# Kernel tuning notes

Measured on AMD Instinct MI355X. Metric: run time of the kernel, lower is better.

The kernel has to match this reference:

```python
import jax, jax.numpy as jnp
import numpy as np
import math

NUM_BINS = 10
TAIL_BOUND = 5.0
FILTER_CHANNELS = 192
KERNEL_SIZE = 3
N_LAYERS = 3
HALF = 1
MIN_BIN = 1e-3
MIN_DERIV = 1e-3


def conv1d(x, w, b, dilation=1, groups=1, padding=0):
    # x: [B,C,T], w: [O, C//groups, K]
    y = jax.lax.conv_general_dilated(
        x, w, window_strides=(1,), padding=[(padding, padding)],
        rhs_dilation=(dilation,), dimension_numbers=('NCH', 'OIH', 'NCH'),
        feature_group_count=groups)
    return y + b[None, :, None]


def ln_channels(x, g, b, eps=1e-5):
    # LayerNorm over channel dim (VITS modules.LayerNorm)
    m = jnp.mean(x, axis=1, keepdims=True)
    v = jnp.mean((x - m) ** 2, axis=1, keepdims=True)
    return g[None, :, None] * (x - m) * jax.lax.rsqrt(v + eps) + b[None, :, None]


def rq_spline(x1, uw, uh, ud):
    # piecewise rational-quadratic transform with linear tails (Durkan et al.)
    # x1: [B,1,T]; uw,uh: [B,1,T,K]; ud: [B,1,T,K-1]
    K = NUM_BINS
    tb = TAIL_BOUND
    inside = (x1 >= -tb) & (x1 <= tb)

    const = math.log(math.exp(1.0 - MIN_DERIV) - 1.0)  # softplus^-1(1-min_d)
    ud = jnp.pad(ud, [(0, 0)] * (ud.ndim - 1) + [(1, 1)], constant_values=const)

    widths = jax.nn.softmax(uw, axis=-1)
    widths = MIN_BIN + (1.0 - MIN_BIN * K) * widths
    cumw = jnp.pad(jnp.cumsum(widths, -1), [(0, 0)] * (uw.ndim - 1) + [(1, 0)])
    cumw = 2.0 * tb * cumw - tb
    cumw = cumw.at[..., 0].set(-tb).at[..., -1].set(tb)
    widths = cumw[..., 1:] - cumw[..., :-1]

    heights = jax.nn.softmax(uh, axis=-1)
    heights = MIN_BIN + (1.0 - MIN_BIN * K) * heights
    cumh = jnp.pad(jnp.cumsum(heights, -1), [(0, 0)] * (uh.ndim - 1) + [(1, 0)])
    cumh = 2.0 * tb * cumh - tb
    cumh = cumh.at[..., 0].set(-tb).at[..., -1].set(tb)
    heights = cumh[..., 1:] - cumh[..., :-1]

    derivs = MIN_DERIV + jax.nn.softplus(ud)  # [..., K+1]

    xin = jnp.clip(x1, -tb, tb)  # clamp so out-of-range lanes stay finite
    locs = cumw.at[..., -1].add(1e-6)
    bin_idx = jnp.clip(jnp.sum((xin[..., None] >= locs).astype(jnp.int32), -1) - 1, 0, K - 1)

    def take(a):
        return jnp.take_along_axis(a, bin_idx[..., None], axis=-1)[..., 0]

    icw = take(cumw)
    iw = take(widths)
    ich = take(cumh)
    ih = take(heights)
    d_l = take(derivs[..., :-1])
    d_r = take(derivs[..., 1:])
    delta = ih / iw

    theta = (xin - icw) / iw
    t1m = theta * (1.0 - theta)
    numerator = ih * (delta * theta * theta + d_l * t1m)
    denominator = delta + (d_l + d_r - 2.0 * delta) * t1m
    y = ich + numerator / denominator
    dnum = (delta * delta) * (d_r * theta * theta + 2.0 * delta * t1m + d_l * (1.0 - theta) ** 2)
    lad = jnp.log(dnum) - 2.0 * jnp.log(denominator)

    out = jnp.where(inside, y, x1)       # linear tails: identity outside
    lad = jnp.where(inside, lad, 0.0)
    return out, lad


def reference(x, x_mask, pre_w, pre_b, sep_w, sep_b, pw_w, pw_b,
              ln1_g, ln1_b, ln2_g, ln2_b, proj_w, proj_b):
    x0, x1 = x[:, :HALF], x[:, HALF:]
    h = conv1d(x0, pre_w, pre_b)
    # DDSConv (dilated depth-separable conv stack), p_dropout=0
    for i in range(N_LAYERS):
        d = KERNEL_SIZE ** i
        pad = (KERNEL_SIZE * d - d) // 2
        y = conv1d(h * x_mask, sep_w[i], sep_b[i], dilation=d,
                   groups=FILTER_CHANNELS, padding=pad)
        y = jax.nn.gelu(ln_channels(y, ln1_g[i], ln1_b[i]), approximate=False)
        y = conv1d(y, pw_w[i], pw_b[i])
        y = jax.nn.gelu(ln_channels(y, ln2_g[i], ln2_b[i]), approximate=False)
        h = h + y
    h = h * x_mask
    h = conv1d(h, proj_w, proj_b) * x_mask  # [B, half*(3K-1), T]
    b, c, t = x0.shape
    h = h.reshape(b, c, -1, t).transpose(0, 1, 3, 2)  # [B, half, T, 3K-1]
    scale = math.sqrt(FILTER_CHANNELS)
    uw = h[..., :NUM_BINS] / scale
    uh = h[..., NUM_BINS:2 * NUM_BINS] / scale
    ud = h[..., 2 * NUM_BINS:]
    x1o, lad = rq_spline(x1, uw, uh, ud)
    out = jnp.concatenate([x0, x1o], axis=1) * x_mask
    logdet = jnp.sum(lad * x_mask, axis=(1, 2))
    return out, logdet


def setup_inputs() -> dict:
    key = jax.random.key(0)
    ks = jax.random.split(key, 8)
    B, T, C, L, K = 64, 4096, FILTER_CHANNELS, N_LAYERS, KERNEL_SIZE
    return {
        'x': jax.random.normal(ks[0], (B, 2, T), jnp.float32),
        'x_mask': jnp.ones((B, 1, T), jnp.float32),
        'pre_w': jax.random.normal(ks[1], (C, 1, 1), jnp.float32) * 0.1,
        'pre_b': jnp.zeros((C,), jnp.float32),
        'sep_w': jax.random.normal(ks[2], (L, C, 1, K), jnp.float32) * 0.1,
        'sep_b': jnp.zeros((L, C), jnp.float32),
        'pw_w': jax.random.normal(ks[3], (L, C, C, 1), jnp.float32) * (1.0 / np.sqrt(C).astype(np.float32)),
        'pw_b': jnp.zeros((L, C), jnp.float32),
        'ln1_g': jnp.ones((L, C), jnp.float32),
        'ln1_b': jnp.zeros((L, C), jnp.float32),
        'ln2_g': jnp.ones((L, C), jnp.float32),
        'ln2_b': jnp.zeros((L, C), jnp.float32),
        'proj_w': jax.random.normal(ks[4], (HALF * (3 * NUM_BINS - 1), C, 1), jnp.float32) * 0.01,
        'proj_b': jnp.zeros((HALF * (3 * NUM_BINS - 1),), jnp.float32),
    }
```

## Files before the change

### kernel.cpp

```cpp
#include <hip/hip_runtime.h>
#include <stdint.h>

#define TT_ 4096
#define CC_ 192
#define TILE_ 64
#define HALO_ 13
#define TW_ 90
#define HS_ 100
#define YTS_ 200
#define NT_ 512

typedef float f32x4 __attribute__((ext_vector_type(4)));
typedef short s16x4 __attribute__((ext_vector_type(4)));
typedef short s16x8 __attribute__((ext_vector_type(8)));
typedef uint32_t ui32x2 __attribute__((ext_vector_type(2)));
typedef uint32_t ui32x4 __attribute__((ext_vector_type(4)));

__device__ __forceinline__ float bf2f(short s){
  uint32_t u = ((uint32_t)(uint16_t)s) << 16;
  float f; __builtin_memcpy(&f, &u, 4); return f;
}
__device__ __forceinline__ float bfhalf(uint32_t u, int hi){
  uint32_t v = hi ? (u & 0xFFFF0000u) : (u << 16);
  float f; __builtin_memcpy(&f, &v, 4); return f;
}
__device__ __forceinline__ short f2bf(float f){
  uint32_t u; __builtin_memcpy(&u, &f, 4);
  u += 0x7FFFu + ((u >> 16) & 1u);
  return (short)(u >> 16);
}
__device__ __forceinline__ uint32_t fbits(float f){
  uint32_t u; __builtin_memcpy(&u, &f, 4); return u;
}
__device__ __forceinline__ uint32_t pk_trunc(float lo, float hi){
  return __builtin_amdgcn_perm(fbits(hi), fbits(lo), 0x07060302u);
}
__device__ __forceinline__ uint32_t rne_u(float f){
  uint32_t u = fbits(f);
  return u + 0x7FFFu + ((u >> 16) & 1u);
}
__device__ __forceinline__ uint32_t pk_rne(float lo, float hi){
  return __builtin_amdgcn_perm(rne_u(hi), rne_u(lo), 0x07060302u);
}
__device__ __forceinline__ float gelu_f(float x){
  float t = x*x;
  float p = x*__builtin_fmaf(t, 0.0713548162f, 1.5957691216f);
  float e = __expf(-p);
  return x * __builtin_amdgcn_rcpf(1.0f + e);
}
__device__ __forceinline__ int ytix(int row, int col){
  return row*YTS_ + ((((col >> 3) ^ (row & 3)) << 3) | (col & 7));
}

template<int D>
__device__ __forceinline__ void dw_pass(const short* __restrict__ Hs, short* __restrict__ YTs,
    const float* __restrict__ sw, const float* __restrict__ sb,
    int jlo, int jhi, int tid){
  constexpr int WO = (D==9) ? 16 : 8;
  constexpr int NU = (D==9) ? 20 : 12;
  for (int g = tid; g < 96*12; g += NT_){
    int cg = g % 96, jg = g / 96;
    int j0 = jg*8;
    if (j0 + 8 <= jlo || j0 >= jhi) continue;
    int c0 = cg*2;
    uint32_t wpa[NU], wpb[NU];
    {
      const uint32_t* ra = (const uint32_t*)(Hs + (c0+0)*HS_ + j0 - WO);
      const uint32_t* rb = (const uint32_t*)(Hs + (c0+1)*HS_ + j0 - WO);
      #pragma unroll
      for (int u = 0; u < NU/2; ++u){
        ui32x2 ta = *(const ui32x2*)(ra + u*2);
        ui32x2 tb = *(const ui32x2*)(rb + u*2);
        wpa[u*2] = ta[0]; wpa[u*2+1] = ta[1];
        wpb[u*2] = tb[0]; wpb[u*2+1] = tb[1];
      }
    }
    float w0a = sw[c0*3+0], w1a = sw[c0*3+1], w2a = sw[c0*3+2], bav = sb[c0];
    float w0b = sw[c0*3+3], w1b = sw[c0*3+4], w2b = sw[c0*3+5], bbv = sb[c0+1];
    #pragma unroll
    for (int j = 0; j < 8; ++j){
      int h0 = WO + j - D, h1 = WO + j, h2 = WO + j + D;
      float va = __builtin_fmaf(w0a, bfhalf(wpa[h0>>1], h0&1),
                 __builtin_fmaf(w1a, bfhalf(wpa[h1>>1], h1&1),
                 __builtin_fmaf(w2a, bfhalf(wpa[h2>>1], h2&1), bav)));
      float vb = __builtin_fmaf(w0b, bfhalf(wpb[h0>>1], h0&1),
                 __builtin_fmaf(w1b, bfhalf(wpb[h1>>1], h1&1),
                 __builtin_fmaf(w2b, bfhalf(wpb[h2>>1], h2&1), bbv)));
      *(uint32_t*)(YTs + ytix(j0+j, c0)) = pk_trunc(va, vb);
    }
  }
}

__device__ __forceinline__ void ln_stats(const short* __restrict__ YTs, float* __restrict__ SM,
                                         float* __restrict__ SR, int jlo, int jhi, int tid){
  if (tid < 384){
    int row = tid >> 2, qtr = tid & 3;
    if (row >= jlo && row < jhi){
      float s0 = 0.f, s1 = 0.f, q0 = 0.f, q1 = 0.f;
      #pragma unroll
      for (int u=0;u<6;++u){
        s16x8 v = *(const s16x8*)(YTs + ytix(row, qtr*48 + u*8));
        #pragma unroll
        for (int e=0;e<4;e++){ float f=bf2f(v[e]); s0 += f; q0 = __builtin_fmaf(f,f,q0); }
        #pragma unroll
        for (int e=4;e<8;e++){ float f=bf2f(v[e]); s1 += f; q1 = __builtin_fmaf(f,f,q1); }
      }
      float s = s0+s1, q = q0+q1;
      s += __shfl_xor(s,1); q += __shfl_xor(q,1);
      s += __shfl_xor(s,2); q += __shfl_xor(q,2);
      if (qtr==0){
        float mean = s*(1.f/192.f);
        float var = fmaxf(q*(1.f/192.f) - mean*mean, 0.f);
        SM[row]=mean; SR[row]=rsqrtf(var+1e-5f);
      }
    }
  }
}

__global__ __launch_bounds__(512, 4)
void convflow_main(
    const float* __restrict__ x, const float* __restrict__ xmask,
    const float* __restrict__ pre_w, const float* __restrict__ pre_b,
    const float* __restrict__ sep_w, const float* __restrict__ sep_b,
    const float* __restrict__ pw_b,
    const float* __restrict__ ln1_g, const float* __restrict__ ln1_b,
    const float* __restrict__ ln2_g, const float* __restrict__ ln2_b,
    const float* __restrict__ proj_b,
    const short* __restrict__ Wbf, const short* __restrict__ Pbf,
    float* __restrict__ out, float* __restrict__ part)
{
  __shared__ __align__(16) char smem_raw[78592];
  float* MB = (float*)(smem_raw + 0);
  float* XB = (float*)(smem_raw + 640);
  float* SM = (float*)(smem_raw + 1024);
  float* SR = (float*)(smem_raw + 1408);
  short* H  = (short*)(smem_raw + 1792);
  short* YT = (short*)(smem_raw + 40192);
  float* HP = (float*)(smem_raw + 65792);

  const int tid = threadIdx.x;
  const int b = blockIdx.y, tile = blockIdx.x;
  const int t0 = tile*TILE_ - HALO_;

  for (int idx = tid; idx < 160; idx += NT_){
    int j = idx - 16; int t = t0 + j;
    float m = 0.f;
    if (j >= 0 && j < TW_ && t >= 0 && t < TT_) m = xmask[b*TT_ + t];
    MB[idx] = m;
  }
  if (tid < 96){
    int t = t0 + tid; float v = 0.f;
    if (tid < TW_ && t >= 0 && t < TT_) v = x[(b*2)*TT_ + t];
    XB[tid] = v;
  }
  __syncthreads();

  for (int g = tid; g < CC_*24; g += NT_){
    int jq = g % 24, c = g / 24;
    float w = pre_w[c], bb = pre_b[c];
    int j0 = jq*4;
    float v0 = (w*XB[j0+0] + bb)*MB[16+j0+0];
    float v1 = (w*XB[j0+1] + bb)*MB[16+j0+1];
    float v2 = (w*XB[j0+2] + bb)*MB[16+j0+2];
    float v3 = (w*XB[j0+3] + bb)*MB[16+j0+3];
    ui32x2 o; o[0] = pk_rne(v0, v1); o[1] = pk_rne(v2, v3);
    *(ui32x2*)(H + c*HS_ + j0) = o;
  }
  __syncthreads();

  #pragma unroll 1
  for (int li = 0; li < 3; ++li){
    const int jlo = (li==0) ? 1 : ((li==1) ? 4 : 13);
    const int jhi = (li==0) ? 89 : ((li==1) ? 86 : 77);
    const float* sw = sep_w + li*CC_*3;
    const float* sb = sep_b + li*CC_;

    if (li == 0)      dw_pass<1>(H, YT, sw, sb, jlo, jhi, tid);
    else if (li == 1) dw_pass<3>(H, YT, sw, sb, jlo, jhi, tid);
    else              dw_pass<9>(H, YT, sw, sb, jlo, jhi, tid);
    __syncthreads();

    ln_stats(YT, SM, SR, jlo, jhi, tid); __syncthreads();

    {
      const float* g1 = ln1_g + li*CC_;
      const float* b1 = ln1_b + li*CC_;
      for (int g = tid; g < 96*24; g += NT_){
        int ch = g % 24, row = g / 24;
        short* p = YT + ytix(row, ch*8);
        if (row >= jlo && row < jhi){
          float m = SM[row], r = SR[row];
          s16x8 v = *(s16x8*)p;
          f32x4 ga = *(const f32x4*)&g1[ch*8], gb = *(const f32x4*)&g1[ch*8+4];
          f32x4 ba = *(const f32x4*)&b1[ch*8], bb = *(const f32x4*)&b1[ch*8+4];
          float ov[8];
          #pragma unroll
          for (int e=0;e<4;e++){
            float val = (bf2f(v[e]) - m)*r*ga[e] + ba[e];
            ov[e] = gelu_f(val);
          }
          #pragma unroll
          for (int e=4;e<8;e++){
            float val = (bf2f(v[e]) - m)*r*gb[e-4] + bb[e-4];
            ov[e] = gelu_f(val);
          }
          ui32x4 o;
          #pragma unroll
          for (int e=0;e<4;e++) o[e] = pk_trunc(ov[2*e], ov[2*e+1]);
          *(ui32x4*)p = o;
        } else {
          ui32x4 z = {0u,0u,0u,0u};
          *(ui32x4*)p = z;
        }
      }
    }
    __syncthreads();

    {
      int w = tid >> 6, lane = tid & 63, l16 = lane & 15, q = lane >> 4;
      int Mh = w & 3, Nh = w >> 2;
      f32x4 acc[3][3];
      #pragma unroll
      for (int r=0;r<3;r++)
        #pragma unroll
        for (int s=0;s<3;s++){ f32x4 z = {0.f,0.f,0.f,0.f}; acc[r][s] = z; }
      const short* Wl = Wbf + li*CC_*CC_;
      #pragma unroll
      for (int kk=0;kk<6;++kk){
        s16x8 bv[3], av[3];
        #pragma unroll
        for (int s=0;s<3;++s)
          bv[s] = *(const s16x8*)&YT[ytix((Nh*3+s)*16 + l16, kk*32 + q*8)];
        #pragma unroll
        for (int r=0;r<3;++r)
          av[r] = *(const s16x8*)&Wl[((Mh*3+r)*16 + l16)*CC_ + kk*32 + q*8];
        #pragma unroll
        for (int r=0;r<3;++r)
          #pragma unroll
          for (int s=0;s<3;++s)
            acc[r][s] = __builtin_amdgcn_mfma_f32_16x16x32_bf16(av[r], bv[s], acc[r][s], 0, 0, 0);
      }
      __syncthreads();
      #pragma unroll
      for (int r=0;r<3;++r){
        int m0 = (Mh*3+r)*16 + q*4;
        f32x4 bias = *(const f32x4*)&pw_b[li*CC_ + m0];
        #pragma unroll
        for (int s=0;s<3;++s){
          int n = (Nh*3+s)*16 + l16;
          ui32x2 ov;
          ov[0] = pk_trunc(acc[r][s][0]+bias[0], acc[r][s][1]+bias[1]);
          ov[1] = pk_trunc(acc[r][s][2]+bias[2], acc[r][s][3]+bias[3]);
          *(ui32x2*)(YT + ytix(n, m0)) = ov;
        }
      }
      __syncthreads();
    }

    ln_stats(YT, SM, SR, jlo, jhi, tid); __syncthreads();

    {
      const float* g2 = ln2_g + li*CC_;
      const float* b2 = ln2_b + li*CC_;
      for (int g = tid; g < 24*48; g += NT_){
        int cgp = g % 48, jg = g / 48;
        int j0 = jg*4, c0 = cgp*4;
        if (j0 + 4 <= jlo || j0 >= jhi) continue;
        f32x4 mv = *(f32x4*)&SM[j0], rv = *(f32x4*)&SR[j0];
        f32x4 mk = *(f32x4*)&MB[16 + j0];
        f32x4 gv = *(const f32x4*)&g2[c0], bv = *(const f32x4*)&b2[c0];
        s16x4 yr[4];
        #pragma unroll
        for (int jj=0;jj<4;++jj) yr[jj] = *(s16x4*)(YT + ytix(j0+jj, c0));
        #pragma unroll
        for (int cc=0;cc<4;++cc){
          short* hp_ = H + (c0+cc)*HS_ + j0;
          s16x4 hv = *(s16x4*)hp_;
          float hf[4];
          #pragma unroll
          for (int jj=0;jj<4;++jj){
            int j = j0 + jj;
            float val = (bf2f(yr[jj][cc]) - mv[jj])*rv[jj]*gv[cc] + bv[cc];
            float hn = (bf2f(hv[jj]) + gelu_f(val))*mk[jj];
            bool ok = (j >= jlo) && (j < jhi);
            hf[jj] = ok ? hn : bf2f(hv[jj]);
          }
          ui32x2 o; o[0] = pk_rne(hf[0], hf[1]); o[1] = pk_rne(hf[2], hf[3]);
          *(ui32x2*)hp_ = o;
        }
      }
    }
    __syncthreads();
  }

  {
    int w = tid >> 6;
    if (w < 4){
      int lane = tid & 63, l16 = lane & 15, q = lane >> 4;
      int mt = w >> 1, ntp = w & 1;
      f32x4 pacc[2];
      { f32x4 z = {0.f,0.f,0.f,0.f}; pacc[0] = z; pacc[1] = z; }
      #pragma unroll
      for (int kk=0;kk<6;++kk){
        s16x8 a = *(const s16x8*)&Pbf[(mt*16 + l16)*CC_ + kk*32 + q*8];
        #pragma unroll
        for (int s=0;s<2;++s){
          int n = (ntp*2+s)*16 + l16;
          s16x8 bvv;
          #pragma unroll
          for (int i=0;i<8;++i)
            bvv[i] = H[(kk*32 + q*8 + i)*HS_ + HALO_ + n];
          pacc[s] = __builtin_amdgcn_mfma_f32_16x16x32_bf16(a, bvv, pacc[s], 0, 0, 0);
        }
      }
      #pragma unroll
      for (int s=0;s<2;++s)
        #pragma unroll
        for (int e=0;e<4;e++){
          int m = mt*16 + q*4 + e;
          if (m < 29){
            int n = (ntp*2+s)*16 + l16;
            HP[n*33 + m] = (pacc[s][e] + proj_b[m]) * MB[16 + HALO_ + n];
          }
        }
    }
  }
  __syncthreads();

  if (tid < 64){
    const int n = tid;
    const int tg = tile*TILE_ + n;
    const float msk = MB[16 + HALO_ + n];
    const float* hp = &HP[n*33];
    const float inv_s = 0.07216878364870323f;
    float uw[10], uh[10], ud9[9];
    #pragma unroll
    for (int k=0;k<10;k++){ uw[k] = hp[k]*inv_s; uh[k] = hp[10+k]*inv_s; }
    #pragma unroll
    for (int k=0;k<9;k++) ud9[k] = hp[20+k];

    float cumw[11], cumh[11];
    {
      float mx = uw[0];
      #pragma unroll
      for (int k=1;k<10;k++) mx = fmaxf(mx, uw[k]);
      float ex[10]; float ss = 0.f;
      #pragma unroll
      for (int k=0;k<10;k++){ ex[k] = __expf(uw[k]-mx); ss += ex[k]; }
      float inv = 1.0f/ss;
      cumw[0] = -5.f; float cw = 0.f;
      #pragma unroll
      for (int k=0;k<10;k++){ float wk = 0.001f + 0.99f*(ex[k]*inv); cw += wk; cumw[k+1] = 10.f*cw - 5.f; }
      cumw[10] = 5.f;
    }
    {
      float mx = uh[0];
      #pragma unroll
      for (int k=1;k<10;k++) mx = fmaxf(mx, uh[k]);
      float ex[10]; float ss = 0.f;
      #pragma unroll
      for (int k=0;k<10;k++){ ex[k] = __expf(uh[k]-mx); ss += ex[k]; }
      float inv = 1.0f/ss;
      cumh[0] = -5.f; float ch = 0.f;
      #pragma unroll
      for (int k=0;k<10;k++){ float hk = 0.001f + 0.99f*(ex[k]*inv); ch += hk; cumh[k+1] = 10.f*ch - 5.f; }
      cumh[10] = 5.f;
    }
    float dv[11];
    dv[0] = 1.0f; dv[10] = 1.0f;
    #pragma unroll
    for (int k=0;k<9;k++){
      float u = ud9[k];
      float sp = (u > 15.f) ? u : log1pf(__expf(u));
      dv[k+1] = 0.001f + sp;
    }

    const float x1 = x[(b*2+1)*TT_ + tg];
    const float xin = fminf(fmaxf(x1, -5.f), 5.f);
    int cnt = 0;
    #pragma unroll
    for (int k=0;k<11;k++){
      float lk = cumw[k] + ((k==10) ? 1e-6f : 0.f);
      cnt += (xin >= lk) ? 1 : 0;
    }
    int bin = cnt - 1;
    bin = (bin < 0) ? 0 : ((bin > 9) ? 9 : bin);

    float icw=0.f, iw=1.f, ich=0.f, ih=1.f, dl=1.f, dr=1.f;
    #pragma unroll
    for (int k=0;k<10;k++){
      if (bin == k){
        icw = cumw[k]; iw = cumw[k+1]-cumw[k];
        ich = cumh[k]; ih = cumh[k+1]-cumh[k];
        dl = dv[k]; dr = dv[k+1];
      }
    }
    float delta = ih/iw;
    float th = (xin - icw)/iw;
    float t1m = th*(1.f-th);
    float num = ih*(delta*th*th + dl*t1m);
    float den = delta + (dl + dr - 2.f*delta)*t1m;
    float yv = ich + num/den;
    float omt = 1.f - th;
    float dnum = delta*delta*(dr*th*th + 2.f*delta*t1m + dl*omt*omt);
    float lad = logf(dnum) - 2.f*logf(den);
    bool inside = (x1 >= -5.f) && (x1 <= 5.f);
    float outv = inside ? yv : x1;
    float ladv = inside ? lad : 0.f;

    out[(b*2)*TT_ + tg]   = x[(b*2)*TT_ + tg] * msk;
    out[(b*2+1)*TT_ + tg] = outv * msk;

    float lsum = ladv * msk;
    #pragma unroll
    for (int off = 32; off > 0; off >>= 1) lsum += __shfl_xor(lsum, off);
    if (tid == 0) part[b*64 + tile] = lsum;
  }
}

__global__ void convflow_pre(const float* __restrict__ pw_w, const float* __restrict__ proj_w,
                             short* __restrict__ Wbf, short* __restrict__ Pbf){
  int idx = blockIdx.x*256 + threadIdx.x;
  if (idx < 110592) Wbf[idx] = f2bf(pw_w[idx]);
  if (idx < 32*192){
    int m = idx / 192, k = idx - m*192;
    Pbf[idx] = (m < 29) ? f2bf(proj_w[m*192 + k]) : (short)0;
  }
}

__global__ void convflow_logdet(const float* __restrict__ part, float* __restrict__ out){
  int bb = threadIdx.x;
  if (bb < 64){
    float s = 0.f;
    for (int k=0;k<64;k++) s += part[bb*64 + k];
    out[524288 + bb] = s;
  }
}

extern "C" void kernel_launch(void* const* d_in, const int* in_sizes, int n_in,
                              void* d_out, int out_size, void* d_ws, size_t ws_size,
                              hipStream_t stream) {
  const float* x      = (const float*)d_in[0];
  const float* xmask  = (const float*)d_in[1];
  const float* pre_w  = (const float*)d_in[2];
  const float* pre_b  = (const float*)d_in[3];
  const float* sep_w  = (const float*)d_in[4];
  const float* sep_b  = (const float*)d_in[5];
  const float* pw_w   = (const float*)d_in[6];
  const float* pw_b   = (const float*)d_in[7];
  const float* ln1_g  = (const float*)d_in[8];
  const float* ln1_b  = (const float*)d_in[9];
  const float* ln2_g  = (const float*)d_in[10];
  const float* ln2_b  = (const float*)d_in[11];
  const float* proj_w = (const float*)d_in[12];
  const float* proj_b = (const float*)d_in[13];

  short* Wbf = (short*)d_ws;
  short* Pbf = (short*)((char*)d_ws + 221184);
  float* part = (float*)((char*)d_ws + 233472);
  float* out = (float*)d_out;

  convflow_pre<<<432, 256, 0, stream>>>(pw_w, proj_w, Wbf, Pbf);
  dim3 grid(64, 64);
  convflow_main<<<grid, NT_, 0, stream>>>(x, xmask, pre_w, pre_b, sep_w, sep_b, pw_b,
                                          ln1_g, ln1_b, ln2_g, ln2_b, proj_b,
                                          Wbf, Pbf, out, part);
  convflow_logdet<<<1, 64, 0, stream>>>(part, out);
}
```

Measured before the change: 591.8 us.

## Store residual H tile time-major with swizzled layout for vectorized access

```diff
diff --git a/kernel.cpp b/kernel.cpp
--- a/kernel.cpp
+++ b/kernel.cpp
@@ -6,7 +6,6 @@
 #define TILE_ 64
 #define HALO_ 13
 #define TW_ 90
-#define HS_ 100
 #define YTS_ 200
 #define NT_ 512
 
@@ -20,10 +19,6 @@
   uint32_t u = ((uint32_t)(uint16_t)s) << 16;
   float f; __builtin_memcpy(&f, &u, 4); return f;
 }
-__device__ __forceinline__ float bfhalf(uint32_t u, int hi){
-  uint32_t v = hi ? (u & 0xFFFF0000u) : (u << 16);
-  float f; __builtin_memcpy(&f, &v, 4); return f;
-}
 __device__ __forceinline__ short f2bf(float f){
   uint32_t u; __builtin_memcpy(&u, &f, 4);
   u += 0x7FFFu + ((u >> 16) & 1u);
@@ -56,38 +51,29 @@
 __device__ __forceinline__ void dw_pass(const short* __restrict__ Hs, short* __restrict__ YTs,
     const float* __restrict__ sw, const float* __restrict__ sb,
     int jlo, int jhi, int tid){
-  constexpr int WO = (D==9) ? 16 : 8;
-  constexpr int NU = (D==9) ? 20 : 12;
-  for (int g = tid; g < 96*12; g += NT_){
-    int cg = g % 96, jg = g / 96;
-    int j0 = jg*8;
-    if (j0 + 8 <= jlo || j0 >= jhi) continue;
-    int c0 = cg*2;
-    uint32_t wpa[NU], wpb[NU];
-    {
-      const uint32_t* ra = (const uint32_t*)(Hs + (c0+0)*HS_ + j0 - WO);
-      const uint32_t* rb = (const uint32_t*)(Hs + (c0+1)*HS_ + j0 - WO);
-      #pragma unroll
-      for (int u = 0; u < NU/2; ++u){
-        ui32x2 ta = *(const ui32x2*)(ra + u*2);
-        ui32x2 tb = *(const ui32x2*)(rb + u*2);
-        wpa[u*2] = ta[0]; wpa[u*2+1] = ta[1];
-        wpb[u*2] = tb[0]; wpb[u*2+1] = tb[1];
-      }
-    }
-    float w0a = sw[c0*3+0], w1a = sw[c0*3+1], w2a = sw[c0*3+2], bav = sb[c0];
-    float w0b = sw[c0*3+3], w1b = sw[c0*3+4], w2b = sw[c0*3+5], bbv = sb[c0+1];
-    #pragma unroll
-    for (int j = 0; j < 8; ++j){
-      int h0 = WO + j - D, h1 = WO + j, h2 = WO + j + D;
-      float va = __builtin_fmaf(w0a, bfhalf(wpa[h0>>1], h0&1),
-                 __builtin_fmaf(w1a, bfhalf(wpa[h1>>1], h1&1),
-                 __builtin_fmaf(w2a, bfhalf(wpa[h2>>1], h2&1), bav)));
-      float vb = __builtin_fmaf(w0b, bfhalf(wpb[h0>>1], h0&1),
-                 __builtin_fmaf(w1b, bfhalf(wpb[h1>>1], h1&1),
-                 __builtin_fmaf(w2b, bfhalf(wpb[h2>>1], h2&1), bbv)));
-      *(uint32_t*)(YTs + ytix(j0+j, c0)) = pk_trunc(va, vb);
-    }
+  for (int g = 24*jlo + tid; g < 24*jhi; g += NT_){
+    int gr = g % 24;
+    int j  = g / 24;
+    int c0 = gr*8;
+    s16x8 t0 = *(const s16x8*)(Hs + ytix(j-D, c0));
+    s16x8 t1 = *(const s16x8*)(Hs + ytix(j,   c0));
+    s16x8 t2 = *(const s16x8*)(Hs + ytix(j+D, c0));
+    float wv[24], bw[8];
+    #pragma unroll
+    for (int u=0;u<6;++u) *(f32x4*)&wv[u*4] = *(const f32x4*)&sw[c0*3 + u*4];
+    *(f32x4*)&bw[0] = *(const f32x4*)&sb[c0];
+    *(f32x4*)&bw[4] = *(const f32x4*)&sb[c0+4];
+    float v[8];
+    #pragma unroll
+    for (int e=0;e<8;++e){
+      v[e] = __builtin_fmaf(wv[e*3+0], bf2f(t0[e]),
+             __builtin_fmaf(wv[e*3+1], bf2f(t1[e]),
+             __builtin_fmaf(wv[e*3+2], bf2f(t2[e]), bw[e])));
+    }
+    ui32x4 o;
+    #pragma unroll
+    for (int e=0;e<4;++e) o[e] = pk_trunc(v[2*e], v[2*e+1]);
+    *(ui32x4*)(YTs + ytix(j, c0)) = o;
   }
 }
 
@@ -155,16 +141,21 @@
   }
   __syncthreads();
 
-  for (int g = tid; g < CC_*24; g += NT_){
-    int jq = g % 24, c = g / 24;
-    float w = pre_w[c], bb = pre_b[c];
-    int j0 = jq*4;
-    float v0 = (w*XB[j0+0] + bb)*MB[16+j0+0];
-    float v1 = (w*XB[j0+1] + bb)*MB[16+j0+1];
-    float v2 = (w*XB[j0+2] + bb)*MB[16+j0+2];
-    float v3 = (w*XB[j0+3] + bb)*MB[16+j0+3];
-    ui32x2 o; o[0] = pk_rne(v0, v1); o[1] = pk_rne(v2, v3);
-    *(ui32x2*)(H + c*HS_ + j0) = o;
+  for (int g = tid; g < 96*24; g += NT_){
+    int gr = g % 24, j = g / 24;
+    int c = gr*8;
+    float xv = XB[j], mv = MB[16+j];
+    f32x4 wa = *(const f32x4*)&pre_w[c], wb = *(const f32x4*)&pre_w[c+4];
+    f32x4 ba = *(const f32x4*)&pre_b[c], bb = *(const f32x4*)&pre_b[c+4];
+    float v[8];
+    #pragma unroll
+    for (int e=0;e<4;++e) v[e]   = (wa[e]*xv + ba[e])*mv;
+    #pragma unroll
+    for (int e=0;e<4;++e) v[4+e] = (wb[e]*xv + bb[e])*mv;
+    ui32x4 o;
+    #pragma unroll
+    for (int e=0;e<4;++e) o[e] = pk_rne(v[2*e], v[2*e+1]);
+    *(ui32x4*)(H + ytix(j, c)) = o;
   }
   __syncthreads();
 
@@ -262,32 +253,30 @@
     {
       const float* g2 = ln2_g + li*CC_;
       const float* b2 = ln2_b + li*CC_;
-      for (int g = tid; g < 24*48; g += NT_){
-        int cgp = g % 48, jg = g / 48;
-        int j0 = jg*4, c0 = cgp*4;
-        if (j0 + 4 <= jlo || j0 >= jhi) continue;
-        f32x4 mv = *(f32x4*)&SM[j0], rv = *(f32x4*)&SR[j0];
-        f32x4 mk = *(f32x4*)&MB[16 + j0];
-        f32x4 gv = *(const f32x4*)&g2[c0], bv = *(const f32x4*)&b2[c0];
-        s16x4 yr[4];
-        #pragma unroll
-        for (int jj=0;jj<4;++jj) yr[jj] = *(s16x4*)(YT + ytix(j0+jj, c0));
-        #pragma unroll
-        for (int cc=0;cc<4;++cc){
-          short* hp_ = H + (c0+cc)*HS_ + j0;
-          s16x4 hv = *(s16x4*)hp_;
-          float hf[4];
-          #pragma unroll
-          for (int jj=0;jj<4;++jj){
-            int j = j0 + jj;
-            float val = (bf2f(yr[jj][cc]) - mv[jj])*rv[jj]*gv[cc] + bv[cc];
-            float hn = (bf2f(hv[jj]) + gelu_f(val))*mk[jj];
-            bool ok = (j >= jlo) && (j < jhi);
-            hf[jj] = ok ? hn : bf2f(hv[jj]);
-          }
-          ui32x2 o; o[0] = pk_rne(hf[0], hf[1]); o[1] = pk_rne(hf[2], hf[3]);
-          *(ui32x2*)hp_ = o;
-        }
+      for (int g = 24*jlo + tid; g < 24*jhi; g += NT_){
+        int gr = g % 24, row = g / 24;
+        int c0 = gr*8;
+        float m = SM[row], r = SR[row], mk = MB[16+row];
+        s16x8 y = *(const s16x8*)(YT + ytix(row, c0));
+        short* hp_ = H + ytix(row, c0);
+        s16x8 hv = *(const s16x8*)hp_;
+        f32x4 ga = *(const f32x4*)&g2[c0], gb = *(const f32x4*)&g2[c0+4];
+        f32x4 ba = *(const f32x4*)&b2[c0], bb = *(const f32x4*)&b2[c0+4];
+        float hf[8];
+        #pragma unroll
+        for (int e=0;e<4;++e){
+          float val = (bf2f(y[e]) - m)*r*ga[e] + ba[e];
+          hf[e] = (bf2f(hv[e]) + gelu_f(val))*mk;
+        }
+        #pragma unroll
+        for (int e=4;e<8;++e){
+          float val = (bf2f(y[e]) - m)*r*gb[e-4] + bb[e-4];
+          hf[e] = (bf2f(hv[e]) + gelu_f(val))*mk;
+        }
+        ui32x4 o;
+        #pragma unroll
+        for (int e=0;e<4;++e) o[e] = pk_rne(hf[2*e], hf[2*e+1]);
+        *(ui32x4*)hp_ = o;
       }
     }
     __syncthreads();
@@ -306,10 +295,7 @@
         #pragma unroll
         for (int s=0;s<2;++s){
           int n = (ntp*2+s)*16 + l16;
-          s16x8 bvv;
-          #pragma unroll
-          for (int i=0;i<8;++i)
-            bvv[i] = H[(kk*32 + q*8 + i)*HS_ + HALO_ + n];
+          s16x8 bvv = *(const s16x8*)(H + ytix(HALO_ + n, kk*32 + q*8));
           pacc[s] = __builtin_amdgcn_mfma_f32_16x16x32_bf16(a, bvv, pacc[s], 0, 0, 0);
         }
       }
```

Result: slower. 623.9 us (+5.4%).
